# Kernel optimization log

Measured on AMD Instinct MI355X. Metric: run time of the kernel, lower is better.

## Reference

```python
import jax, jax.numpy as jnp
import numpy as np
from jax import lax


def setup_inputs() -> dict:
    key = jax.random.key(0)
    k1, k2 = jax.random.split(key)
    B, T, C, U, W = 8, 4096, 512, 512, 2
    inputs = jax.random.normal(k1, (B, T, C), dtype=jnp.float32)
    kernel = jax.random.normal(k2, (W, C, 3 * U), dtype=jnp.float32) * (1.0 / np.sqrt(W * C))
    bias = jnp.zeros((3 * U,), dtype=jnp.float32)
    return {"inputs": inputs, "kernel": kernel, "bias": bias}


def _fo_pool(x, f):
    # x, f: [B, T, U]; c_t = f_t * c_{t-1} + (1 - f_t) * x_t, c_0 = 0
    xT = jnp.swapaxes(x, 0, 1)  # [T, B, U]
    fT = jnp.swapaxes(f, 0, 1)
    c0 = jnp.zeros(x.shape[:1] + x.shape[2:], dtype=x.dtype)  # [B, U]

    def step(c, fx):
        ft, xt = fx
        c = ft * c + (1.0 - ft) * xt
        return c, c

    _, cT = lax.scan(step, c0, (fT, xT))
    return jnp.swapaxes(cT, 0, 1)  # [B, T, U]


def reference(inputs, kernel, bias):
    # Conv1D, padding='same', stride=1, NWC layout
    gates = lax.conv_general_dilated(
        inputs, kernel, window_strides=(1,), padding='SAME',
        dimension_numbers=('NWC', 'WIO', 'NWC')) + bias  # [B, T, 3U]
    x, forget, output = jnp.split(gates, 3, axis=-1)
    x = jnp.tanh(x)
    forget = jax.nn.sigmoid(forget)
    c = _fo_pool(x, forget)
    h = jax.nn.sigmoid(output) * c
    return h
```

## Files before the change

### kernel.cpp

```cpp
#include <hip/hip_runtime.h>

typedef unsigned short u16;
typedef unsigned int u32;
typedef _Float16 f16;
typedef __attribute__((ext_vector_type(8))) _Float16 half8;
typedef __attribute__((ext_vector_type(2))) __fp16 fp16x2;
typedef __attribute__((ext_vector_type(4))) float float4_;
typedef __attribute__((ext_vector_type(4))) unsigned short ushort4_;
typedef __attribute__((ext_vector_type(4))) unsigned int u32x4;

union hu { f16 h; u16 u; };

__device__ __forceinline__ u32 pkrtz(float a, float b) {
    fp16x2 t = __builtin_amdgcn_cvt_pkrtz(a, b);
    union { fp16x2 h; u32 u; } cv; cv.h = t;
    return cv.u;
}

__device__ __forceinline__ void gl16(const u16* g, u16* l) {
    __builtin_amdgcn_global_load_lds(
        (const __attribute__((address_space(1))) void*)g,
        (__attribute__((address_space(3))) void*)l, 16, 0, 0);
}

#define Bsz 8
#define Tsz 4096
#define Csz 512
#define Usz 512
#define NG  1536
#define KK  1024
#define MM  32768
#define NCH 128
#define CHL 32

__global__ void prep_a(const float* __restrict__ in, u16* __restrict__ A16) {
    int gid = blockIdx.x * 256 + threadIdx.x;
    int idx8 = gid * 8;
    int c8 = idx8 & 511;
    int row = idx8 >> 9;
    int b = (u32)row / 4097u;
    int t = row - b * 4097;
    u32x4 w;
    if (t == Tsz) {
        w = (u32x4)0;
    } else {
        const float* p = in + ((size_t)(b * Tsz + t) << 9) + c8;
        float4_ v0 = *(const float4_*)p;
        float4_ v1 = *(const float4_*)(p + 4);
        w.x = pkrtz(v0.x, v0.y); w.y = pkrtz(v0.z, v0.w);
        w.z = pkrtz(v1.x, v1.y); w.w = pkrtz(v1.z, v1.w);
    }
    *(u32x4*)(A16 + idx8) = w;
}

__global__ void prep_k(const float* __restrict__ kern, u16* __restrict__ KT) {
    __shared__ u16 t[64][70];
    const int k0 = blockIdx.x * 64;
    const int n0 = blockIdx.y * 64;
    const int tid = threadIdx.x;
    #pragma unroll
    for (int it = 0; it < 16; ++it) {
        int s = it * 256 + tid;
        int r = s >> 6;
        int c = s & 63;
        float v = kern[(size_t)(k0 + r) * NG + n0 + c];
        hu cv; cv.h = (f16)v;
        t[c][r] = cv.u;
    }
    __syncthreads();
    #pragma unroll
    for (int it = 0; it < 4; ++it) {
        int s = it * 256 + tid;
        int n = s >> 4;
        int kq = (s & 15) * 4;
        ushort4_ w;
        w.x = t[n][kq]; w.y = t[n][kq + 1]; w.z = t[n][kq + 2]; w.w = t[n][kq + 3];
        *(ushort4_*)(KT + (size_t)(n0 + n) * KK + k0 + kq) = w;
    }
}

#define LDS_T 8192

__device__ __forceinline__ void stageA3(const u16* __restrict__ A16, u16* dst,
                                        int arow_base, int kin, int tid, int lane) {
    #pragma unroll
    for (int it = 0; it < 2; ++it) {
        int s = it * 512 + tid;
        int row = s >> 2, c = s & 3;
        gl16(A16 + (((size_t)(arow_base + row)) << 9) + kin + c * 8, dst + (s - lane) * 8);
    }
}

__device__ __forceinline__ void stageB3(const u16* __restrict__ KT, u16* dst,
                                        int n0, int kk, int tid, int lane) {
    #pragma unroll
    for (int it = 0; it < 2; ++it) {
        int s = it * 512 + tid;
        int row = s >> 2, c = s & 3;
        gl16(KT + (((size_t)(n0 + row)) << 10) + kk + c * 8, dst + (s - lane) * 8);
    }
}

__global__ __launch_bounds__(512, 2) void gemm_gates(
    const u16* __restrict__ A16, const u16* __restrict__ KT,
    const float* __restrict__ bias,
    u16* __restrict__ X, u16* __restrict__ F, float* __restrict__ O)
{
    __shared__ u16 lA[3 * LDS_T];
    __shared__ u16 lB[3 * LDS_T];

    const int tid  = threadIdx.x;
    const int lane = tid & 63;
    const int wave = tid >> 6;

    const int orig = blockIdx.x;
    const int wg = (orig & 7) * 96 + (orig >> 3);
    const int nb = wg % 6;
    const int mb = wg / 6;
    const int m0 = mb * 256;
    const int n0 = nb * 256;
    const int b  = m0 >> 12;
    const int t0 = m0 & 4095;
    const int arow0 = b * (Tsz + 1) + t0;

    float4_ acc[8][4];
    #pragma unroll
    for (int i = 0; i < 8; ++i)
        #pragma unroll
        for (int j = 0; j < 4; ++j) acc[i][j] = (float4_)0.0f;

    const int wm = (wave >> 2) * 128;
    const int wn = (wave & 3) * 64;
    const int fr = lane & 15;
    const int fq = lane >> 4;

    stageA3(A16, lA, arow0, 0, tid, lane);
    stageB3(KT, lB, n0, 0, tid, lane);
    stageA3(A16, lA + LDS_T, arow0, 32, tid, lane);
    stageB3(KT, lB + LDS_T, n0, 32, tid, lane);

    int buf = 0;
    #pragma unroll 1
    for (int kt = 0; kt < 32; ++kt) {
        if (kt < 31) asm volatile("s_waitcnt vmcnt(4)" ::: "memory");
        else         asm volatile("s_waitcnt vmcnt(0)" ::: "memory");
        __builtin_amdgcn_s_barrier();

        const u16* a  = lA + buf * LDS_T;
        const u16* bs = lB + buf * LDS_T;
        const int nbuf = (buf >= 1) ? buf - 1 : 2;
        const int kt2 = kt + 2;
        const int kk2 = kt2 * 32;
        const bool st = kt2 < 32;

        half8 fa[4], fb[4];
        #pragma unroll
        for (int j = 0; j < 4; ++j)
            fa[j] = *(const half8*)(a + (wm + j * 16 + fr) * 32 + fq * 8);
        #pragma unroll
        for (int n = 0; n < 4; ++n)
            fb[n] = *(const half8*)(bs + (wn + n * 16 + fr) * 32 + fq * 8);
        if (st) stageA3(A16, lA + nbuf * LDS_T, arow0 + (kk2 >> 9), kk2 & 511, tid, lane);
        __builtin_amdgcn_sched_barrier(0);
        __builtin_amdgcn_s_setprio(1);
        #pragma unroll
        for (int mi = 0; mi < 4; ++mi)
            #pragma unroll
            for (int ni = 0; ni < 4; ++ni)
                acc[mi][ni] = __builtin_amdgcn_mfma_f32_16x16x32_f16(fa[mi], fb[ni], acc[mi][ni], 0, 0, 0);
        __builtin_amdgcn_s_setprio(0);

        half8 fa2[4];
        #pragma unroll
        for (int j = 0; j < 4; ++j)
            fa2[j] = *(const half8*)(a + (wm + 64 + j * 16 + fr) * 32 + fq * 8);
        if (st) stageB3(KT, lB + nbuf * LDS_T, n0, kk2, tid, lane);
        __builtin_amdgcn_sched_barrier(0);
        __builtin_amdgcn_s_setprio(1);
        #pragma unroll
        for (int mi = 0; mi < 4; ++mi)
            #pragma unroll
            for (int ni = 0; ni < 4; ++ni)
                acc[4 + mi][ni] = __builtin_amdgcn_mfma_f32_16x16x32_f16(fa2[mi], fb[ni], acc[4 + mi][ni], 0, 0, 0);
        __builtin_amdgcn_s_setprio(0);

        buf = (buf == 2) ? 0 : buf + 1;
    }

    const int plane = nb >> 1;
    const int rq = fq * 4;
    #pragma unroll
    for (int mi = 0; mi < 8; ++mi)
        #pragma unroll
        for (int ni = 0; ni < 4; ++ni) {
            const int gm = m0 + wm + mi * 16 + rq;
            const int gn = n0 + wn + ni * 16 + fr;
            const float bv = bias[gn];
            const int cp = gn & 511;
            #pragma unroll
            for (int r2 = 0; r2 < 4; ++r2) {
                float v = acc[mi][ni][r2] + bv;
                if (plane == 0) {
                    float res = 1.0f - 2.0f / (__expf(2.0f * v) + 1.0f);
                    hu cv; cv.h = (f16)res;
                    X[(size_t)(gm + r2) * Usz + cp] = cv.u;
                } else if (plane == 1) {
                    float res = 1.0f / (1.0f + __expf(-v));
                    hu cv; cv.h = (f16)res;
                    F[(size_t)(gm + r2) * Usz + cp] = cv.u;
                } else {
                    float res = 1.0f / (1.0f + __expf(-v));
                    O[(size_t)(gm + r2) * Usz + cp] = res;
                }
            }
        }
}

__device__ __forceinline__ float4_ x4(const u16* p) {
    ushort4_ xr = *(const ushort4_*)p;
    float4_ xv;
    #pragma unroll
    for (int j = 0; j < 4; ++j) { hu cv; cv.u = xr[j]; xv[j] = (float)cv.h; }
    return xv;
}

__global__ void scan_chunk(const u16* __restrict__ F, const u16* __restrict__ X,
                           float* __restrict__ CA, float* __restrict__ CB) {
    int g = blockIdx.x * 256 + threadIdx.x;
    int u4 = (g & 127) * 4;
    int bc = g >> 7;
    size_t base = (size_t)bc * CHL * Usz + u4;
    float4_ c = (float4_)0.0f, A = (float4_)1.0f;
    for (int i = 0; i < CHL; ++i) {
        float4_ fv = x4(F + base + (size_t)i * Usz);
        float4_ xv = x4(X + base + (size_t)i * Usz);
        c = fv * c + (1.0f - fv) * xv;
        A = A * fv;
    }
    *(float4_*)(CA + (size_t)bc * Usz + u4) = A;
    *(float4_*)(CB + (size_t)bc * Usz + u4) = c;
}

__global__ void scan_prefix(const float* __restrict__ CA, const float* __restrict__ CB,
                            float* __restrict__ CS) {
    int g = blockIdx.x * 256 + threadIdx.x;
    int u = g & 511;
    int b = g >> 9;
    float c = 0.0f;
    #pragma unroll 16
    for (int ch = 0; ch < NCH; ++ch) {
        int idx = (b * NCH + ch) * Usz + u;
        CS[idx] = c;
        c = CA[idx] * c + CB[idx];
    }
}

__global__ void scan_final(const u16* __restrict__ F, const u16* __restrict__ X,
                           const float* __restrict__ CS, float* __restrict__ out) {
    int g = blockIdx.x * 256 + threadIdx.x;
    int u4 = (g & 127) * 4;
    int bc = g >> 7;
    size_t base = (size_t)bc * CHL * Usz + u4;
    float4_ c = *(const float4_*)(CS + (size_t)bc * Usz + u4);
    for (int i = 0; i < CHL; ++i) {
        float4_ fv = x4(F + base + (size_t)i * Usz);
        float4_ xv = x4(X + base + (size_t)i * Usz);
        c = fv * c + (1.0f - fv) * xv;
        float4_ ov = *(const float4_*)(out + base + (size_t)i * Usz);
        *(float4_*)(out + base + (size_t)i * Usz) = ov * c;
    }
}

extern "C" void kernel_launch(void* const* d_in, const int* in_sizes, int n_in,
                              void* d_out, int out_size, void* d_ws, size_t ws_size,
                              hipStream_t stream) {
    const float* in   = (const float*)d_in[0];
    const float* kern = (const float*)d_in[1];
    const float* bias = (const float*)d_in[2];
    float* out = (float*)d_out;
    char* ws = (char*)d_ws;

    const size_t A16_B  = (size_t)Bsz * (Tsz + 1) * Csz * 2;
    const size_t OFF_KT = A16_B;
    const size_t OFF_F  = OFF_KT + (size_t)NG * KK * 2;
    const size_t OFF_X  = OFF_F + (size_t)MM * Usz * 2;
    const size_t NEED   = OFF_X + (size_t)MM * Usz * 2;

    if (ws_size < NEED) return;

    u16*   A16 = (u16*)ws;
    u16*   KT  = (u16*)(ws + OFF_KT);
    u16*   Fh  = (u16*)(ws + OFF_F);
    u16*   Xb  = (u16*)(ws + OFF_X);
    const size_t CH = (size_t)Bsz * NCH * Usz;
    float* CA = (float*)ws;
    float* CB = CA + CH;
    float* CS = CB + CH;

    prep_a<<<(int)(A16_B / 16 / 256), 256, 0, stream>>>(in, A16);
    prep_k<<<dim3(KK / 64, NG / 64), 256, 0, stream>>>(kern, KT);
    gemm_gates<<<(MM / 256) * (NG / 256), 512, 0, stream>>>(A16, KT, bias, Xb, Fh, out);
    scan_chunk<<<Bsz * NCH * Usz / 4 / 256, 256, 0, stream>>>(Fh, Xb, CA, CB);
    scan_prefix<<<Bsz * Usz / 256, 256, 0, stream>>>(CA, CB, CS);
    scan_final<<<Bsz * NCH * Usz / 4 / 256, 256, 0, stream>>>(Fh, Xb, CS, out);
}
```

Before: 302.0 us.

## Restructure GEMM main loop into 64-wide K steps with swizzled LDS and quadrant pipelining

Replaces the triple-buffered 32-wide K loop with double-buffered 64-wide K tiles. Each tile is split into halves that are staged between four quadrant MFMA phases in a ping-pong schedule, with barriers between phases. LDS rows now use an XOR swizzle on 16-byte chunks to avoid bank conflicts on fragment reads, and loop-carried buffer indexing is replaced by a fully unrolled two-tile iteration. The aim is better overlap of global-to-LDS loads with MFMA work and fewer LDS bank conflicts, at the cost of many more barriers and more fragile vmcnt accounting.

```diff
diff --git a/kernel.cpp b/kernel.cpp
--- a/kernel.cpp
+++ b/kernel.cpp
@@ -79,35 +79,47 @@
     }
 }
 
-#define LDS_T 8192
-
-__device__ __forceinline__ void stageA3(const u16* __restrict__ A16, u16* dst,
-                                        int arow_base, int kin, int tid, int lane) {
+#define ABUF 16384
+
+__device__ __forceinline__ void stageAh(const u16* __restrict__ A16, u16* dst,
+                                        int arow0, int kt, int h, int tid, int lane) {
+    const int tap = kt >> 3;
+    const int kin = (kt & 7) * 64;
     #pragma unroll
     for (int it = 0; it < 2; ++it) {
         int s = it * 512 + tid;
-        int row = s >> 2, c = s & 3;
-        gl16(A16 + (((size_t)(arow_base + row)) << 9) + kin + c * 8, dst + (s - lane) * 8);
-    }
-}
-
-__device__ __forceinline__ void stageB3(const u16* __restrict__ KT, u16* dst,
-                                        int n0, int kk, int tid, int lane) {
+        int rl = s >> 3, p = s & 7;
+        int c = p ^ (rl & 7);
+        gl16(A16 + (((size_t)(arow0 + h * 128 + rl + tap)) << 9) + kin + c * 8,
+             dst + h * 8192 + (s - lane) * 8);
+    }
+}
+
+__device__ __forceinline__ void stageBh(const u16* __restrict__ KT, u16* dst,
+                                        int n0, int kt, int h, int tid, int lane) {
+    const int kk = kt * 64;
     #pragma unroll
     for (int it = 0; it < 2; ++it) {
         int s = it * 512 + tid;
-        int row = s >> 2, c = s & 3;
-        gl16(KT + (((size_t)(n0 + row)) << 10) + kk + c * 8, dst + (s - lane) * 8);
-    }
-}
+        int rl = s >> 3, p = s & 7;
+        int c = p ^ (rl & 7);
+        gl16(KT + (((size_t)(n0 + h * 128 + rl)) << 10) + kk + c * 8,
+             dst + h * 8192 + (s - lane) * 8);
+    }
+}
+
+#define FRAG_A(buf, mh, j, ks) \
+    (*(const half8*)((buf) + (wm + (mh)*64 + (j)*16 + fr) * 64 + ((((ks)*4 + fq) ^ swz) * 8)))
+#define FRAG_B(buf, nh, n, ks) \
+    (*(const half8*)((buf) + (wn + (nh)*32 + (n)*16 + fr) * 64 + ((((ks)*4 + fq) ^ swz) * 8)))
 
 __global__ __launch_bounds__(512, 2) void gemm_gates(
     const u16* __restrict__ A16, const u16* __restrict__ KT,
     const float* __restrict__ bias,
     u16* __restrict__ X, u16* __restrict__ F, float* __restrict__ O)
 {
-    __shared__ u16 lA[3 * LDS_T];
-    __shared__ u16 lB[3 * LDS_T];
+    __shared__ u16 lA[2 * ABUF];
+    __shared__ u16 lB[2 * ABUF];
 
     const int tid  = threadIdx.x;
     const int lane = tid & 63;
@@ -133,58 +145,162 @@
     const int wn = (wave & 3) * 64;
     const int fr = lane & 15;
     const int fq = lane >> 4;
-
-    stageA3(A16, lA, arow0, 0, tid, lane);
-    stageB3(KT, lB, n0, 0, tid, lane);
-    stageA3(A16, lA + LDS_T, arow0, 32, tid, lane);
-    stageB3(KT, lB + LDS_T, n0, 32, tid, lane);
-
-    int buf = 0;
+    const int swz = fr & 7;
+
+    stageAh(A16, lA, arow0, 0, 0, tid, lane);
+    stageAh(A16, lA, arow0, 0, 1, tid, lane);
+    stageBh(KT, lB, n0, 0, 0, tid, lane);
+    stageBh(KT, lB, n0, 0, 1, tid, lane);
+    asm volatile("" ::: "memory");
+    stageBh(KT, lB + ABUF, n0, 1, 0, tid, lane);
+    stageBh(KT, lB + ABUF, n0, 1, 1, tid, lane);
+    asm volatile("s_waitcnt vmcnt(0)" ::: "memory");
+    __builtin_amdgcn_s_barrier();
+
+    half8 fa0[4][2], fa1[4][2], fb0[2][2], fb1[2][2];
+
     #pragma unroll 1
-    for (int kt = 0; kt < 32; ++kt) {
-        if (kt < 31) asm volatile("s_waitcnt vmcnt(4)" ::: "memory");
-        else         asm volatile("s_waitcnt vmcnt(0)" ::: "memory");
-        __builtin_amdgcn_s_barrier();
-
-        const u16* a  = lA + buf * LDS_T;
-        const u16* bs = lB + buf * LDS_T;
-        const int nbuf = (buf >= 1) ? buf - 1 : 2;
-        const int kt2 = kt + 2;
-        const int kk2 = kt2 * 32;
-        const bool st = kt2 < 32;
-
-        half8 fa[4], fb[4];
-        #pragma unroll
-        for (int j = 0; j < 4; ++j)
-            fa[j] = *(const half8*)(a + (wm + j * 16 + fr) * 32 + fq * 8);
-        #pragma unroll
-        for (int n = 0; n < 4; ++n)
-            fb[n] = *(const half8*)(bs + (wn + n * 16 + fr) * 32 + fq * 8);
-        if (st) stageA3(A16, lA + nbuf * LDS_T, arow0 + (kk2 >> 9), kk2 & 511, tid, lane);
-        __builtin_amdgcn_sched_barrier(0);
-        __builtin_amdgcn_s_setprio(1);
-        #pragma unroll
-        for (int mi = 0; mi < 4; ++mi)
-            #pragma unroll
-            for (int ni = 0; ni < 4; ++ni)
-                acc[mi][ni] = __builtin_amdgcn_mfma_f32_16x16x32_f16(fa[mi], fb[ni], acc[mi][ni], 0, 0, 0);
-        __builtin_amdgcn_s_setprio(0);
-
-        half8 fa2[4];
-        #pragma unroll
-        for (int j = 0; j < 4; ++j)
-            fa2[j] = *(const half8*)(a + (wm + 64 + j * 16 + fr) * 32 + fq * 8);
-        if (st) stageB3(KT, lB + nbuf * LDS_T, n0, kk2, tid, lane);
-        __builtin_amdgcn_sched_barrier(0);
-        __builtin_amdgcn_s_setprio(1);
-        #pragma unroll
-        for (int mi = 0; mi < 4; ++mi)
-            #pragma unroll
-            for (int ni = 0; ni < 4; ++ni)
-                acc[4 + mi][ni] = __builtin_amdgcn_mfma_f32_16x16x32_f16(fa2[mi], fb[ni], acc[4 + mi][ni], 0, 0, 0);
-        __builtin_amdgcn_s_setprio(0);
-
-        buf = (buf == 2) ? 0 : buf + 1;
+    for (int i = 0; i < 8; ++i) {
+        const int tOdd = 2 * i + 1;
+        const int tNx0 = 2 * i + 2;
+        const int tNx1 = 2 * i + 3;
+        const bool more = (i < 7);
+
+        #pragma unroll
+        for (int j = 0; j < 4; ++j) { fa0[j][0] = FRAG_A(lA, 0, j, 0); fa0[j][1] = FRAG_A(lA, 0, j, 1); }
+        #pragma unroll
+        for (int n = 0; n < 2; ++n) { fb0[n][0] = FRAG_B(lB, 0, n, 0); fb0[n][1] = FRAG_B(lB, 0, n, 1); }
+        stageAh(A16, lA + ABUF, arow0, tOdd, 0, tid, lane);
+        __builtin_amdgcn_s_barrier();
+        asm volatile("s_waitcnt lgkmcnt(0)" ::: "memory");
+        __builtin_amdgcn_sched_barrier(0);
+        __builtin_amdgcn_s_setprio(1);
+        #pragma unroll
+        for (int ks = 0; ks < 2; ++ks)
+            #pragma unroll
+            for (int mi = 0; mi < 4; ++mi)
+                #pragma unroll
+                for (int ni = 0; ni < 2; ++ni)
+                    acc[mi][ni] = __builtin_amdgcn_mfma_f32_16x16x32_f16(fa0[mi][ks], fb0[ni][ks], acc[mi][ni], 0, 0, 0);
+        __builtin_amdgcn_s_setprio(0);
+        __builtin_amdgcn_s_barrier();
+
+        #pragma unroll
+        for (int n = 0; n < 2; ++n) { fb1[n][0] = FRAG_B(lB, 1, n, 0); fb1[n][1] = FRAG_B(lB, 1, n, 1); }
+        stageAh(A16, lA + ABUF, arow0, tOdd, 1, tid, lane);
+        __builtin_amdgcn_s_barrier();
+        asm volatile("s_waitcnt lgkmcnt(0)" ::: "memory");
+        __builtin_amdgcn_sched_barrier(0);
+        __builtin_amdgcn_s_setprio(1);
+        #pragma unroll
+        for (int ks = 0; ks < 2; ++ks)
+            #pragma unroll
+            for (int mi = 0; mi < 4; ++mi)
+                #pragma unroll
+                for (int ni = 0; ni < 2; ++ni)
+                    acc[mi][ni + 2] = __builtin_amdgcn_mfma_f32_16x16x32_f16(fa0[mi][ks], fb1[ni][ks], acc[mi][ni + 2], 0, 0, 0);
+        __builtin_amdgcn_s_setprio(0);
+        __builtin_amdgcn_s_barrier();
+
+        #pragma unroll
+        for (int j = 0; j < 4; ++j) { fa1[j][0] = FRAG_A(lA, 1, j, 0); fa1[j][1] = FRAG_A(lA, 1, j, 1); }
+        if (more) stageBh(KT, lB, n0, tNx0, 0, tid, lane);
+        __builtin_amdgcn_s_barrier();
+        asm volatile("s_waitcnt lgkmcnt(0)" ::: "memory");
+        __builtin_amdgcn_sched_barrier(0);
+        __builtin_amdgcn_s_setprio(1);
+        #pragma unroll
+        for (int ks = 0; ks < 2; ++ks)
+            #pragma unroll
+            for (int mi = 0; mi < 4; ++mi)
+                #pragma unroll
+                for (int ni = 0; ni < 2; ++ni)
+                    acc[4 + mi][ni] = __builtin_amdgcn_mfma_f32_16x16x32_f16(fa1[mi][ks], fb0[ni][ks], acc[4 + mi][ni], 0, 0, 0);
+        __builtin_amdgcn_s_setprio(0);
+        __builtin_amdgcn_s_barrier();
+
+        if (more) stageBh(KT, lB, n0, tNx0, 1, tid, lane);
+        __builtin_amdgcn_s_barrier();
+        __builtin_amdgcn_s_setprio(1);
+        #pragma unroll
+        for (int ks = 0; ks < 2; ++ks)
+            #pragma unroll
+            for (int mi = 0; mi < 4; ++mi)
+                #pragma unroll
+                for (int ni = 0; ni < 2; ++ni)
+                    acc[4 + mi][ni + 2] = __builtin_amdgcn_mfma_f32_16x16x32_f16(fa1[mi][ks], fb1[ni][ks], acc[4 + mi][ni + 2], 0, 0, 0);
+        __builtin_amdgcn_s_setprio(0);
+        if (more) asm volatile("s_waitcnt vmcnt(4)" ::: "memory");
+        else      asm volatile("s_waitcnt vmcnt(0)" ::: "memory");
+        __builtin_amdgcn_s_barrier();
+
+        #pragma unroll
+        for (int j = 0; j < 4; ++j) { fa0[j][0] = FRAG_A(lA + ABUF, 0, j, 0); fa0[j][1] = FRAG_A(lA + ABUF, 0, j, 1); }
+        #pragma unroll
+        for (int n = 0; n < 2; ++n) { fb0[n][0] = FRAG_B(lB + ABUF, 0, n, 0); fb0[n][1] = FRAG_B(lB + ABUF, 0, n, 1); }
+        if (more) stageAh(A16, lA, arow0, tNx0, 0, tid, lane);
+        __builtin_amdgcn_s_barrier();
+        asm volatile("s_waitcnt lgkmcnt(0)" ::: "memory");
+        __builtin_amdgcn_sched_barrier(0);
+        __builtin_amdgcn_s_setprio(1);
+        #pragma unroll
+        for (int ks = 0; ks < 2; ++ks)
+            #pragma unroll
+            for (int mi = 0; mi < 4; ++mi)
+                #pragma unroll
+                for (int ni = 0; ni < 2; ++ni)
+                    acc[mi][ni] = __builtin_amdgcn_mfma_f32_16x16x32_f16(fa0[mi][ks], fb0[ni][ks], acc[mi][ni], 0, 0, 0);
+        __builtin_amdgcn_s_setprio(0);
+        __builtin_amdgcn_s_barrier();
+
+        #pragma unroll
+        for (int n = 0; n < 2; ++n) { fb1[n][0] = FRAG_B(lB + ABUF, 1, n, 0); fb1[n][1] = FRAG_B(lB + ABUF, 1, n, 1); }
+        if (more) stageAh(A16, lA, arow0, tNx0, 1, tid, lane);
+        __builtin_amdgcn_s_barrier();
+        asm volatile("s_waitcnt lgkmcnt(0)" ::: "memory");
+        __builtin_amdgcn_sched_barrier(0);
+        __builtin_amdgcn_s_setprio(1);
+        #pragma unroll
+        for (int ks = 0; ks < 2; ++ks)
+            #pragma unroll
+            for (int mi = 0; mi < 4; ++mi)
+                #pragma unroll
+                for (int ni = 0; ni < 2; ++ni)
+                    acc[mi][ni + 2] = __builtin_amdgcn_mfma_f32_16x16x32_f16(fa0[mi][ks], fb1[ni][ks], acc[mi][ni + 2], 0, 0, 0);
+        __builtin_amdgcn_s_setprio(0);
+        __builtin_amdgcn_s_barrier();
+
+        #pragma unroll
+        for (int j = 0; j < 4; ++j) { fa1[j][0] = FRAG_A(lA + ABUF, 1, j, 0); fa1[j][1] = FRAG_A(lA + ABUF, 1, j, 1); }
+        if (more) stageBh(KT, lB + ABUF, n0, tNx1, 0, tid, lane);
+        __builtin_amdgcn_s_barrier();
+        asm volatile("s_waitcnt lgkmcnt(0)" ::: "memory");
+        __builtin_amdgcn_sched_barrier(0);
+        __builtin_amdgcn_s_setprio(1);
+        #pragma unroll
+        for (int ks = 0; ks < 2; ++ks)
+            #pragma unroll
+            for (int mi = 0; mi < 4; ++mi)
+                #pragma unroll
+                for (int ni = 0; ni < 2; ++ni)
+                    acc[4 + mi][ni] = __builtin_amdgcn_mfma_f32_16x16x32_f16(fa1[mi][ks], fb0[ni][ks], acc[4 + mi][ni], 0, 0, 0);
+        __builtin_amdgcn_s_setprio(0);
+        __builtin_amdgcn_s_barrier();
+
+        if (more) stageBh(KT, lB + ABUF, n0, tNx1, 1, tid, lane);
+        __builtin_amdgcn_s_barrier();
+        __builtin_amdgcn_s_setprio(1);
+        #pragma unroll
+        for (int ks = 0; ks < 2; ++ks)
+            #pragma unroll
+            for (int mi = 0; mi < 4; ++mi)
+                #pragma unroll
+                for (int ni = 0; ni < 2; ++ni)
+                    acc[4 + mi][ni + 2] = __builtin_amdgcn_mfma_f32_16x16x32_f16(fa1[mi][ks], fb1[ni][ks], acc[4 + mi][ni + 2], 0, 0, 0);
+        __builtin_amdgcn_s_setprio(0);
+        if (more) asm volatile("s_waitcnt vmcnt(4)" ::: "memory");
+        else      asm volatile("s_waitcnt vmcnt(0)" ::: "memory");
+        __builtin_amdgcn_s_barrier();
     }
 
     const int plane = nb >> 1;
```

After: 297.6 us. Within noise of the previous version (-1.5%).
